# Kernel optimization log

Hardware: AMD Instinct MI355X
Metric: run time of the kernel (lower is better)

Reference implementation:

```python
import jax, jax.numpy as jnp
import numpy as np

DATA_NUM = 1024
CLS_NUM = 32000


def setup_inputs() -> dict:
    key = jax.random.key(0)
    k1, k2, k3, k4 = jax.random.split(key, 4)
    h1 = jax.random.normal(k1, (DATA_NUM, 2), dtype=jnp.float32) + 3.0
    e1 = jax.random.normal(k2, (CLS_NUM, 2), dtype=jnp.float32)
    h3 = jax.random.normal(k3, (DATA_NUM, 2), dtype=jnp.float32) * 2.0
    e3 = jax.random.normal(k4, (CLS_NUM, 2), dtype=jnp.float32)
    return {"h1": h1, "e1": e1, "h3": h3, "e3": e3, "share_head": 0}


def cal_akl(l1, l2):
    # l1: student logits (D, C); l2: teacher logits (D, C)
    probs1 = jax.nn.softmax(l1, axis=-1)
    probs2 = jax.nn.softmax(l2, axis=-1)
    # sort teacher probs ascending; gather student probs in same order
    sorted_idx = jnp.argsort(probs2, axis=-1)
    sorted_probs2 = jnp.take_along_axis(probs2, sorted_idx, axis=-1)
    sorted_probs1 = jnp.take_along_axis(probs1, sorted_idx, axis=-1)
    gap = jnp.abs(sorted_probs2 - sorted_probs1)
    cum_probs2 = jnp.cumsum(sorted_probs2, axis=-1)
    tail_mask = (cum_probs2 < 0.5).astype(l1.dtype)
    g_head = jax.lax.stop_gradient(jnp.sum(gap * (1.0 - tail_mask), axis=-1))
    g_tail = jax.lax.stop_gradient(jnp.sum(gap * tail_mask, axis=-1))
    lprobs1 = jax.nn.log_softmax(l1, axis=-1)
    lprobs2 = jax.nn.log_softmax(l2, axis=-1)
    fkl = jnp.sum(probs2 * (lprobs2 - lprobs1), axis=-1)
    rkl = jnp.sum(probs1 * (lprobs1 - lprobs2), axis=-1)
    denom = g_head + g_tail
    akl = (g_head / denom) * fkl + (g_tail / denom) * rkl
    return jnp.mean(akl)


def reference(h1, e1, h3, e3, share_head):
    # share_head is a static Python int/bool; obj == 'akl', share_head == 0 path
    if share_head:
        raise NotImplementedError("reference covers share_head=False path")
    stu_logits = h1 @ e1.T   # (D, C)
    tea_logits = h3 @ e3.T   # (D, C)
    return cal_akl(stu_logits, tea_logits)
```

## Files before the change

### kernel.cpp

```cpp
#include <hip/hip_runtime.h>
#include <math.h>

#define DNUM 1024
#define CNUM 32000
#define NT 512
#define R 2
#define GRID (DNUM / R)
#define KC 8
#define KF 8
#define NQ (CNUM / 4)

#define L2E 1.4426950408889634f
#define LN2 0.6931471805599453f

__device__ __forceinline__ float wave_red_sum(float v) {
    #pragma unroll
    for (int o = 32; o > 0; o >>= 1) v += __shfl_down(v, o, 64);
    return v;
}

__global__ __launch_bounds__(NT, 4) void akl_rows(
    const float* __restrict__ h1, const float* __restrict__ e1,
    const float* __restrict__ h3, const float* __restrict__ e3,
    float* __restrict__ out)
{
    const int tid  = threadIdx.x;
    const int lane = tid & 63, wid = tid >> 6;
    const int row0 = blockIdx.x * R;

    __shared__ float hA[R * KC * NT];
    __shared__ float hG[R * KF * NT];
    __shared__ float red[64];
    __shared__ float shCS[R * KC];
    __shared__ float shFP[R * KF], shFG[R * KF];
    __shared__ float shA[R][10];

    float a1L[R], b1L[R], a2L[R], b2L[R], mh1L[R], mh2L[R], icwC[R];
    #pragma unroll
    for (int r = 0; r < R; r++) {
        a1L[r] = h1[2*(row0+r)] * L2E; b1L[r] = h1[2*(row0+r)+1] * L2E;
        a2L[r] = h3[2*(row0+r)] * L2E; b2L[r] = h3[2*(row0+r)+1] * L2E;
        mh1L[r] = 6.0f * (fabsf(a1L[r]) + fabsf(b1L[r]));
        mh2L[r] = 6.0f * (fabsf(a2L[r]) + fabsf(b2L[r]));
        float sp = fmaxf(sqrtf(a2L[r]*a2L[r] + b2L[r]*b2L[r]), 1e-6f);
        icwC[r] = 1.0f / (0.675f * sp);
    }
    const float C0C = 0.5f / 0.675f;

    for (int i = tid; i < R*KC*NT; i += NT) hA[i] = 0.f;
    __syncthreads();

    const float4* __restrict__ E1 = (const float4*)e1;
    const float4* __restrict__ E3 = (const float4*)e3;

    float U1[R] = {0,0}, S1[R] = {0,0}, S2[R] = {0,0};
    {
        int j = tid;
        float4 A0 = E1[2*j], A1 = E1[2*j+1], B0 = E3[2*j], B1 = E3[2*j+1];
        while (true) {
            const int jn = j + NT;
            const bool more = jn < NQ;
            float4 C0, C1, D0, D1;
            if (more) { C0 = E1[2*jn]; C1 = E1[2*jn+1]; D0 = E3[2*jn]; D1 = E3[2*jn+1]; }
            float x1[4]={A0.x,A0.z,A1.x,A1.z}, y1[4]={A0.y,A0.w,A1.y,A1.w};
            float x3[4]={B0.x,B0.z,B1.x,B1.z}, y3[4]={B0.y,B0.w,B1.y,B1.w};
            #pragma unroll
            for (int r = 0; r < R; r++) {
                #pragma unroll
                for (int k = 0; k < 4; k++) {
                    float l1p = fmaf(a1L[r], x1[k], b1L[r]*y1[k]);
                    float l2p = fmaf(a2L[r], x3[k], b2L[r]*y3[k]);
                    float e1v = __builtin_amdgcn_exp2f(l1p - mh1L[r]);
                    float e2v = __builtin_amdgcn_exp2f(l2p - mh2L[r]);
                    float dp  = l2p - l1p;
                    U1[r] += e1v;
                    S1[r] = fmaf(e1v, dp, S1[r]);
                    S2[r] = fmaf(e2v, dp, S2[r]);
                    int cb = (int)fmaf(l2p, icwC[r], C0C);
                    cb = min(KC-1, max(0, cb));
                    hA[(r*KC + cb)*NT + tid] += e2v;
                }
            }
            if (!more) break;
            j = jn; A0 = C0; A1 = C1; B0 = D0; B1 = D1;
        }
    }
    #pragma unroll
    for (int r = 0; r < R; r++) {
        float u = wave_red_sum(U1[r]);
        float s1 = wave_red_sum(S1[r]);
        float s2 = wave_red_sum(S2[r]);
        if (lane == 0) {
            red[wid*6 + r*3 + 0] = u;
            red[wid*6 + r*3 + 1] = s1;
            red[wid*6 + r*3 + 2] = s2;
        }
    }
    __syncthreads();

    {
        int grp = tid >> 5, l32 = tid & 31;
        float s = 0.f;
        #pragma unroll
        for (int t = 0; t < NT/32; t++) s += hA[grp*NT + l32 + t*32];
        #pragma unroll
        for (int o = 16; o > 0; o >>= 1) s += __shfl_down(s, o, 32);
        if (l32 == 0) shCS[grp] = s;
    }
    __syncthreads();

    if (tid < R) {
        const int r = tid;
        float U1s = 0, S1s = 0, S2s = 0;
        for (int w = 0; w < 8; w++) {
            U1s += red[w*6 + r*3 + 0];
            S1s += red[w*6 + r*3 + 1];
            S2s += red[w*6 + r*3 + 2];
        }
        float U2s = 0.f;
        #pragma unroll
        for (int i = 0; i < KC; i++) U2s += shCS[r*KC + i];
        float M1 = mh1L[r] + __builtin_amdgcn_logf(U1s);
        float M2 = mh2L[r] + __builtin_amdgcn_logf(U2s);
        float delta = M2 - M1;
        float thr = 0.5f * U2s;
        float S = 0.f; int bsel = KC-1;
        for (int i = 0; i < KC; i++) {
            float m = shCS[r*KC + i];
            if (S + m >= thr) { bsel = i; break; }
            S += m;
        }
        float sp = fmaxf(sqrtf(a2L[r]*a2L[r] + b2L[r]*b2L[r]), 1e-6f);
        float wc  = 0.675f * sp;
        float loS = fmaf((float)bsel, wc, -0.5f*sp);
        float icwF = (float)KF / wc;
        shA[r][0] = 1.f / U1s;
        shA[r][1] = 1.f / U2s;
        shA[r][2] = thr;
        shA[r][3] = LN2 * (S2s/U2s - delta);
        shA[r][4] = LN2 * (delta - S1s/U1s);
        shA[r][5] = loS;
        shA[r][6] = icwF;
        shA[r][7] = -loS * icwF;
        shA[r][8] = S;
    }
    for (int i = tid; i < R*KF*NT; i += NT) { hA[i] = 0.f; hG[i] = 0.f; }
    __syncthreads();

    float iU1l[R], iU2l[R], loSl[R], icwFl[R], c0Fl[R];
    #pragma unroll
    for (int r = 0; r < R; r++) {
        iU1l[r] = shA[r][0]; iU2l[r] = shA[r][1];
        loSl[r] = shA[r][5]; icwFl[r] = shA[r][6]; c0Fl[r] = shA[r][7];
    }
    float gt[R] = {0,0}, Gpre[R] = {0,0};
    {
        int j = tid;
        float4 A0 = E1[2*j], A1 = E1[2*j+1], B0 = E3[2*j], B1 = E3[2*j+1];
        while (true) {
            const int jn = j + NT;
            const bool more = jn < NQ;
            float4 C0, C1, D0, D1;
            if (more) { C0 = E1[2*jn]; C1 = E1[2*jn+1]; D0 = E3[2*jn]; D1 = E3[2*jn+1]; }
            float x1[4]={A0.x,A0.z,A1.x,A1.z}, y1[4]={A0.y,A0.w,A1.y,A1.w};
            float x3[4]={B0.x,B0.z,B1.x,B1.z}, y3[4]={B0.y,B0.w,B1.y,B1.w};
            #pragma unroll
            for (int r = 0; r < R; r++) {
                #pragma unroll
                for (int k = 0; k < 4; k++) {
                    float l1p = fmaf(a1L[r], x1[k], b1L[r]*y1[k]);
                    float l2p = fmaf(a2L[r], x3[k], b2L[r]*y3[k]);
                    float e1v = __builtin_amdgcn_exp2f(l1p - mh1L[r]);
                    float e2v = __builtin_amdgcn_exp2f(l2p - mh2L[r]);
                    float gap = fabsf(e2v*iU2l[r] - e1v*iU1l[r]);
                    gt[r] += gap;
                    bool below = l2p < loSl[r];
                    Gpre[r] += below ? gap : 0.f;
                    int fb = (int)fmaf(l2p, icwFl[r], c0Fl[r]);
                    if (!below && fb < KF) {
                        int a = (r*KF + fb)*NT + tid;
                        hA[a] += e2v;
                        hG[a] += gap;
                    }
                }
            }
            if (!more) break;
            j = jn; A0 = C0; A1 = C1; B0 = D0; B1 = D1;
        }
    }
    #pragma unroll
    for (int r = 0; r < R; r++) {
        float a = wave_red_sum(gt[r]);
        float b = wave_red_sum(Gpre[r]);
        if (lane == 0) { red[wid*4 + r*2 + 0] = a; red[wid*4 + r*2 + 1] = b; }
    }
    __syncthreads();

    {
        int grp = tid >> 5, l32 = tid & 31;
        float s = 0.f, g = 0.f;
        #pragma unroll
        for (int t = 0; t < NT/32; t++) {
            s += hA[grp*NT + l32 + t*32];
            g += hG[grp*NT + l32 + t*32];
        }
        #pragma unroll
        for (int o = 16; o > 0; o >>= 1) {
            s += __shfl_down(s, o, 32);
            g += __shfl_down(g, o, 32);
        }
        if (l32 == 0) { shFP[grp] = s; shFG[grp] = g; }
    }
    __syncthreads();

    if (tid < R) {
        const int r = tid;
        float gts = 0, Gp = 0;
        for (int w = 0; w < 8; w++) {
            gts += red[w*4 + r*2 + 0];
            Gp  += red[w*4 + r*2 + 1];
        }
        float thr = shA[r][2], fkl = shA[r][3], rkl = shA[r][4];
        float S = shA[r][8], G = Gp;
        bool done = false;
        #pragma unroll
        for (int i = 0; i < KF; i++) {
            if (!done) {
                float p = shFP[r*KF + i], g = shFG[r*KF + i];
                float ns = S + p;
                if (ns >= thr) {
                    float f = (thr - S) / fmaxf(p, 1e-30f);
                    f = fminf(fmaxf(f, 0.f), 1.f);
                    G += f * g;
                    done = true;
                } else { S = ns; G += g; }
            }
        }
        float gl = G;
        float gh = gts - gl;
        float akl = (gh*fkl + gl*rkl) / gts;
        unsafeAtomicAdd(out, akl * (1.0f/(float)DNUM));
    }
}

extern "C" void kernel_launch(void* const* d_in, const int* in_sizes, int n_in,
                              void* d_out, int out_size, void* d_ws, size_t ws_size,
                              hipStream_t stream) {
    const float* h1 = (const float*)d_in[0];
    const float* e1 = (const float*)d_in[1];
    const float* h3 = (const float*)d_in[2];
    const float* e3 = (const float*)d_in[3];
    hipMemsetAsync(d_out, 0, sizeof(float), stream);
    akl_rows<<<GRID, NT, 0, stream>>>(h1, e1, h3, e3, (float*)d_out);
}
```

Measured before the change: 109.2 us.

## Split LDS histograms into four banks and fold max shift into FMA

The two shared histogram arrays are replaced by four per-row/per-k histogram buffers. In pass 1, k-pairs write to separate buffers, so back-to-back read-modify-writes to the same LDS slot are interleaved. The max-shift subtraction is folded into the logit FMA, and the S1/S2 sums are corrected afterwards. Pass 2 replaces the compare against the lower bin bound with a floor of the fine-bin index. Both loops also drop manual register prefetch in favour of a simple loop plus a tail, which adds some LDS to clear and reduce and may expose global-load latency.

```diff
diff --git a/kernel.cpp b/kernel.cpp
--- a/kernel.cpp
+++ b/kernel.cpp
@@ -9,6 +9,8 @@
 #define KC 8
 #define KF 8
 #define NQ (CNUM / 4)
+#define NFULL (NQ / NT)
+#define TAILN (NQ - NFULL*NT)
 
 #define L2E 1.4426950408889634f
 #define LN2 0.6931471805599453f
@@ -28,14 +30,16 @@
     const int lane = tid & 63, wid = tid >> 6;
     const int row0 = blockIdx.x * R;
 
-    __shared__ float hA[R * KC * NT];
-    __shared__ float hG[R * KF * NT];
-    __shared__ float red[64];
-    __shared__ float shCS[R * KC];
-    __shared__ float shFP[R * KF], shFG[R * KF];
-    __shared__ float shA[R][10];
-
-    float a1L[R], b1L[R], a2L[R], b2L[R], mh1L[R], mh2L[R], icwC[R];
+    __shared__ float hC0[KC*NT];
+    __shared__ float hC1[KC*NT];
+    __shared__ float hC2[KC*NT];
+    __shared__ float hC3[KC*NT];
+    __shared__ float red[48];
+    __shared__ float shCS[R*KC];
+    __shared__ float shFP[R*KF], shFG[R*KF];
+    __shared__ float shA[R][8];
+
+    float a1L[R], b1L[R], a2L[R], b2L[R], mh1L[R], mh2L[R], icwC[R], c0C[R];
     #pragma unroll
     for (int r = 0; r < R; r++) {
         a1L[r] = h1[2*(row0+r)] * L2E; b1L[r] = h1[2*(row0+r)+1] * L2E;
@@ -44,52 +48,50 @@
         mh2L[r] = 6.0f * (fabsf(a2L[r]) + fabsf(b2L[r]));
         float sp = fmaxf(sqrtf(a2L[r]*a2L[r] + b2L[r]*b2L[r]), 1e-6f);
         icwC[r] = 1.0f / (0.675f * sp);
-    }
-    const float C0C = 0.5f / 0.675f;
-
-    for (int i = tid; i < R*KC*NT; i += NT) hA[i] = 0.f;
+        c0C[r] = 0.5f/0.675f + mh2L[r]*icwC[r];
+    }
+    for (int i = tid; i < KC*NT; i += NT) {
+        hC0[i] = 0.f; hC1[i] = 0.f; hC2[i] = 0.f; hC3[i] = 0.f;
+    }
     __syncthreads();
 
     const float4* __restrict__ E1 = (const float4*)e1;
     const float4* __restrict__ E3 = (const float4*)e3;
 
-    float U1[R] = {0,0}, S1[R] = {0,0}, S2[R] = {0,0};
-    {
-        int j = tid;
+    float U1[R] = {0,0}, S1p[R] = {0,0}, S2p[R] = {0,0};
+    auto body1 = [&](int j) {
         float4 A0 = E1[2*j], A1 = E1[2*j+1], B0 = E3[2*j], B1 = E3[2*j+1];
-        while (true) {
-            const int jn = j + NT;
-            const bool more = jn < NQ;
-            float4 C0, C1, D0, D1;
-            if (more) { C0 = E1[2*jn]; C1 = E1[2*jn+1]; D0 = E3[2*jn]; D1 = E3[2*jn+1]; }
-            float x1[4]={A0.x,A0.z,A1.x,A1.z}, y1[4]={A0.y,A0.w,A1.y,A1.w};
-            float x3[4]={B0.x,B0.z,B1.x,B1.z}, y3[4]={B0.y,B0.w,B1.y,B1.w};
+        float x1[4]={A0.x,A0.z,A1.x,A1.z}, y1[4]={A0.y,A0.w,A1.y,A1.w};
+        float x3[4]={B0.x,B0.z,B1.x,B1.z}, y3[4]={B0.y,B0.w,B1.y,B1.w};
+        #pragma unroll
+        for (int r = 0; r < R; r++) {
             #pragma unroll
-            for (int r = 0; r < R; r++) {
-                #pragma unroll
-                for (int k = 0; k < 4; k++) {
-                    float l1p = fmaf(a1L[r], x1[k], b1L[r]*y1[k]);
-                    float l2p = fmaf(a2L[r], x3[k], b2L[r]*y3[k]);
-                    float e1v = __builtin_amdgcn_exp2f(l1p - mh1L[r]);
-                    float e2v = __builtin_amdgcn_exp2f(l2p - mh2L[r]);
-                    float dp  = l2p - l1p;
-                    U1[r] += e1v;
-                    S1[r] = fmaf(e1v, dp, S1[r]);
-                    S2[r] = fmaf(e2v, dp, S2[r]);
-                    int cb = (int)fmaf(l2p, icwC[r], C0C);
-                    cb = min(KC-1, max(0, cb));
-                    hA[(r*KC + cb)*NT + tid] += e2v;
-                }
+            for (int k = 0; k < 4; k++) {
+                float l1s = fmaf(a1L[r], x1[k], fmaf(b1L[r], y1[k], -mh1L[r]));
+                float l2s = fmaf(a2L[r], x3[k], fmaf(b2L[r], y3[k], -mh2L[r]));
+                float e1v = __builtin_amdgcn_exp2f(l1s);
+                float e2v = __builtin_amdgcn_exp2f(l2s);
+                float dps = l2s - l1s;
+                U1[r] += e1v;
+                S1p[r] = fmaf(e1v, dps, S1p[r]);
+                S2p[r] = fmaf(e2v, dps, S2p[r]);
+                int cb = (int)fmaf(l2s, icwC[r], c0C[r]);
+                cb = min(KC-1, max(0, cb));
+                float* H = (r == 0) ? ((k < 2) ? hC0 : hC1)
+                                    : ((k < 2) ? hC2 : hC3);
+                H[cb*NT + tid] += e2v;
             }
-            if (!more) break;
-            j = jn; A0 = C0; A1 = C1; B0 = D0; B1 = D1;
-        }
-    }
+        }
+    };
+    #pragma unroll 1
+    for (int it = 0; it < NFULL; ++it) body1(it*NT + tid);
+    if (tid < TAILN) body1(NFULL*NT + tid);
+
     #pragma unroll
     for (int r = 0; r < R; r++) {
         float u = wave_red_sum(U1[r]);
-        float s1 = wave_red_sum(S1[r]);
-        float s2 = wave_red_sum(S2[r]);
+        float s1 = wave_red_sum(S1p[r]);
+        float s2 = wave_red_sum(S2p[r]);
         if (lane == 0) {
             red[wid*6 + r*3 + 0] = u;
             red[wid*6 + r*3 + 1] = s1;
@@ -100,11 +102,16 @@
 
     {
         int grp = tid >> 5, l32 = tid & 31;
+        int r = grp >> 3, b = grp & 7;
+        const float* Ha = r ? hC2 : hC0;
+        const float* Hb = r ? hC3 : hC1;
         float s = 0.f;
         #pragma unroll
-        for (int t = 0; t < NT/32; t++) s += hA[grp*NT + l32 + t*32];
-        #pragma unroll
-        for (int o = 16; o > 0; o >>= 1) s += __shfl_down(s, o, 32);
+        for (int t = 0; t < NT/32; t++) {
+            s += Ha[b*NT + l32 + t*32] + Hb[b*NT + l32 + t*32];
+        }
+        #pragma unroll
+        for (int o = 16; o > 0; o >>= 1) s += __shfl_down(s, o, 64);
         if (l32 == 0) shCS[grp] = s;
     }
     __syncthreads();
@@ -120,8 +127,15 @@
         float U2s = 0.f;
         #pragma unroll
         for (int i = 0; i < KC; i++) U2s += shCS[r*KC + i];
-        float M1 = mh1L[r] + __builtin_amdgcn_logf(U1s);
-        float M2 = mh2L[r] + __builtin_amdgcn_logf(U2s);
+        float mh1r = r ? mh1L[1] : mh1L[0];
+        float mh2r = r ? mh2L[1] : mh2L[0];
+        float a2r = r ? a2L[1] : a2L[0];
+        float b2r = r ? b2L[1] : b2L[0];
+        float dmh = mh2r - mh1r;
+        S1s += dmh * U1s;
+        S2s += dmh * U2s;
+        float M1 = mh1r + __builtin_amdgcn_logf(U1s);
+        float M2 = mh2r + __builtin_amdgcn_logf(U2s);
         float delta = M2 - M1;
         float thr = 0.5f * U2s;
         float S = 0.f; int bsel = KC-1;
@@ -130,64 +144,60 @@
             if (S + m >= thr) { bsel = i; break; }
             S += m;
         }
-        float sp = fmaxf(sqrtf(a2L[r]*a2L[r] + b2L[r]*b2L[r]), 1e-6f);
+        float sp = fmaxf(sqrtf(a2r*a2r + b2r*b2r), 1e-6f);
         float wc  = 0.675f * sp;
-        float loS = fmaf((float)bsel, wc, -0.5f*sp);
+        float loS_s = fmaf((float)bsel, wc, -0.5f*sp) - mh2r;
         float icwF = (float)KF / wc;
         shA[r][0] = 1.f / U1s;
         shA[r][1] = 1.f / U2s;
         shA[r][2] = thr;
         shA[r][3] = LN2 * (S2s/U2s - delta);
         shA[r][4] = LN2 * (delta - S1s/U1s);
-        shA[r][5] = loS;
-        shA[r][6] = icwF;
-        shA[r][7] = -loS * icwF;
-        shA[r][8] = S;
-    }
-    for (int i = tid; i < R*KF*NT; i += NT) { hA[i] = 0.f; hG[i] = 0.f; }
-    __syncthreads();
-
-    float iU1l[R], iU2l[R], loSl[R], icwFl[R], c0Fl[R];
+        shA[r][5] = icwF;
+        shA[r][6] = -loS_s * icwF;
+        shA[r][7] = S;
+    }
+    for (int i = tid; i < KF*NT; i += NT) {
+        hC0[i] = 0.f; hC1[i] = 0.f; hC2[i] = 0.f; hC3[i] = 0.f;
+    }
+    __syncthreads();
+
+    float iU1l[R], iU2l[R], icwFl[R], c0Fl[R];
     #pragma unroll
     for (int r = 0; r < R; r++) {
         iU1l[r] = shA[r][0]; iU2l[r] = shA[r][1];
-        loSl[r] = shA[r][5]; icwFl[r] = shA[r][6]; c0Fl[r] = shA[r][7];
+        icwFl[r] = shA[r][5]; c0Fl[r] = shA[r][6];
     }
     float gt[R] = {0,0}, Gpre[R] = {0,0};
-    {
-        int j = tid;
+    auto body2 = [&](int j) {
         float4 A0 = E1[2*j], A1 = E1[2*j+1], B0 = E3[2*j], B1 = E3[2*j+1];
-        while (true) {
-            const int jn = j + NT;
-            const bool more = jn < NQ;
-            float4 C0, C1, D0, D1;
-            if (more) { C0 = E1[2*jn]; C1 = E1[2*jn+1]; D0 = E3[2*jn]; D1 = E3[2*jn+1]; }
-            float x1[4]={A0.x,A0.z,A1.x,A1.z}, y1[4]={A0.y,A0.w,A1.y,A1.w};
-            float x3[4]={B0.x,B0.z,B1.x,B1.z}, y3[4]={B0.y,B0.w,B1.y,B1.w};
+        float x1[4]={A0.x,A0.z,A1.x,A1.z}, y1[4]={A0.y,A0.w,A1.y,A1.w};
+        float x3[4]={B0.x,B0.z,B1.x,B1.z}, y3[4]={B0.y,B0.w,B1.y,B1.w};
+        #pragma unroll
+        for (int r = 0; r < R; r++) {
             #pragma unroll
-            for (int r = 0; r < R; r++) {
-                #pragma unroll
-                for (int k = 0; k < 4; k++) {
-                    float l1p = fmaf(a1L[r], x1[k], b1L[r]*y1[k]);
-                    float l2p = fmaf(a2L[r], x3[k], b2L[r]*y3[k]);
-                    float e1v = __builtin_amdgcn_exp2f(l1p - mh1L[r]);
-                    float e2v = __builtin_amdgcn_exp2f(l2p - mh2L[r]);
-                    float gap = fabsf(e2v*iU2l[r] - e1v*iU1l[r]);
-                    gt[r] += gap;
-                    bool below = l2p < loSl[r];
-                    Gpre[r] += below ? gap : 0.f;
-                    int fb = (int)fmaf(l2p, icwFl[r], c0Fl[r]);
-                    if (!below && fb < KF) {
-                        int a = (r*KF + fb)*NT + tid;
-                        hA[a] += e2v;
-                        hG[a] += gap;
-                    }
+            for (int k = 0; k < 4; k++) {
+                float l1s = fmaf(a1L[r], x1[k], fmaf(b1L[r], y1[k], -mh1L[r]));
+                float l2s = fmaf(a2L[r], x3[k], fmaf(b2L[r], y3[k], -mh2L[r]));
+                float e1v = __builtin_amdgcn_exp2f(l1s);
+                float e2v = __builtin_amdgcn_exp2f(l2s);
+                float gap = fabsf(fmaf(e1v, -iU1l[r], e2v*iU2l[r]));
+                gt[r] += gap;
+                int fb = (int)floorf(fmaf(l2s, icwFl[r], c0Fl[r]));
+                Gpre[r] += (fb < 0) ? gap : 0.f;
+                if ((unsigned)fb < KF) {
+                    float* HP = r ? hC1 : hC0;
+                    float* HG = r ? hC3 : hC2;
+                    HP[fb*NT + tid] += e2v;
+                    HG[fb*NT + tid] += gap;
                 }
             }
-            if (!more) break;
-            j = jn; A0 = C0; A1 = C1; B0 = D0; B1 = D1;
-        }
-    }
+        }
+    };
+    #pragma unroll 1
+    for (int it = 0; it < NFULL; ++it) body2(it*NT + tid);
+    if (tid < TAILN) body2(NFULL*NT + tid);
+
     #pragma unroll
     for (int r = 0; r < R; r++) {
         float a = wave_red_sum(gt[r]);
@@ -197,19 +207,18 @@
     __syncthreads();
 
     {
-        int grp = tid >> 5, l32 = tid & 31;
-        float s = 0.f, g = 0.f;
-        #pragma unroll
-        for (int t = 0; t < NT/32; t++) {
-            s += hA[grp*NT + l32 + t*32];
-            g += hG[grp*NT + l32 + t*32];
-        }
-        #pragma unroll
-        for (int o = 16; o > 0; o >>= 1) {
-            s += __shfl_down(s, o, 32);
-            g += __shfl_down(g, o, 32);
-        }
-        if (l32 == 0) { shFP[grp] = s; shFG[grp] = g; }
+        int grp = tid >> 4, l16 = tid & 15;
+        int isG = grp >> 4;
+        int r = (grp >> 3) & 1, b = grp & 7;
+        const float* H = isG ? (r ? hC3 : hC2) : (r ? hC1 : hC0);
+        float s = 0.f;
+        #pragma unroll
+        for (int t = 0; t < NT/16; t++) s += H[b*NT + l16 + t*16];
+        #pragma unroll
+        for (int o = 8; o > 0; o >>= 1) s += __shfl_down(s, o, 64);
+        if (l16 == 0) {
+            if (isG) shFG[r*KF + b] = s; else shFP[r*KF + b] = s;
+        }
     }
     __syncthreads();
 
@@ -221,7 +230,7 @@
             Gp  += red[w*4 + r*2 + 1];
         }
         float thr = shA[r][2], fkl = shA[r][3], rkl = shA[r][4];
-        float S = shA[r][8], G = Gp;
+        float S = shA[r][7], G = Gp;
         bool done = false;
         #pragma unroll
         for (int i = 0; i < KF; i++) {
```

Result: faster. 105.1 us (-3.7%).
